# Optimization experiments

Measured on AMD Instinct MI355X. Metric: run time of the kernel, lower is better.

## Reference

```python
import jax, jax.numpy as jnp
import numpy as np

NUM_PARAMS = 8          # number of generalized coordinates q
DIM = 2 * NUM_PARAMS    # state = (q, q_dot)
HID = 128               # hidden width of the Lagrangian MLP
BATCH = 4096


def _linear_init(key, fan_in, fan_out):
    # torch nn.Linear default init: U(-1/sqrt(fan_in), 1/sqrt(fan_in))
    lim = 1.0 / np.sqrt(fan_in)
    kw, kb = jax.random.split(key)
    W = jax.random.uniform(kw, (fan_out, fan_in), minval=-lim, maxval=lim, dtype=jnp.float32)
    b = jax.random.uniform(kb, (fan_out,), minval=-lim, maxval=lim, dtype=jnp.float32)
    return W, b


def setup_inputs() -> dict:
    key = jax.random.key(0)
    ks = jax.random.split(key, 6)
    W1, b1 = _linear_init(ks[0], DIM, HID)
    W2, b2 = _linear_init(ks[1], HID, HID)
    W3, b3 = _linear_init(ks[2], HID, HID)
    W4, b4 = _linear_init(ks[3], HID, HID)
    W5, b5 = _linear_init(ks[4], HID, 1)
    x = jax.random.normal(ks[5], (BATCH, DIM), dtype=jnp.float32)
    return {"x": x, "W1": W1, "b1": b1, "W2": W2, "b2": b2,
            "W3": W3, "b3": b3, "W4": W4, "b4": b4, "W5": W5, "b5": b5}


def reference(x, W1, b1, W2, b2, W3, b3, W4, b4, W5, b5):
    n = NUM_PARAMS

    def lagrangian(xs):  # xs: (DIM,) -> scalar L
        h = jax.nn.softplus(W1 @ xs + b1)
        h = jax.nn.softplus(W2 @ h + b2)
        h = jax.nn.softplus(W3 @ h + b3)
        h = jax.nn.softplus(W4 @ h + b4)
        return (W5 @ h + b5)[0]

    def per_sample(xs):
        J = jax.grad(lagrangian)(xs)            # (DIM,) = dL/dx
        H = jax.hessian(lagrangian)(xs)         # (DIM, DIM)
        A = J[:n]                               # dL/dq
        B = H[n:, n:]                           # d2L/dq_dot dq_dot
        C = H[n:, :n]                           # d2L/dq_dot dq
        # q_ddot = pinv(B) @ (dL/dq - d2L/dq_dot dq @ q_dot)
        return jnp.linalg.pinv(B) @ (A - C @ xs[n:])

    return jax.vmap(per_sample)(x)              # (BATCH, NUM_PARAMS)
```

## Files before the change

kernel.cpp:

```cpp
#include <hip/hip_runtime.h>
#include <math.h>

#define NPAR 8
#define DIM  16
#define HID  128
#define BATCH 4096
#define VSTRF 132
#define NVEC 9

typedef float v2f __attribute__((ext_vector_type(2)));

__device__ float g_wsf[6*HID*HID + HID*DIM];

__device__ __forceinline__ float sigf(float z){ return 1.0f/(1.0f+__expf(-z)); }
__device__ __forceinline__ float spf(float z){ return fmaxf(z,0.0f)+log1pf(__expf(-fabsf(z))); }
__device__ __forceinline__ int posf(int jo, int kr){
  return (((kr>>6)*16 + ((kr&63)>>2))*4 + (jo>>5))*128 + (jo&31)*4 + (kr&3);
}

__global__ void pack_weights(const float* __restrict__ W1, const float* __restrict__ W2,
                             const float* __restrict__ W3, const float* __restrict__ W4) {
  int t = blockIdx.x*blockDim.x + threadIdx.x;
  if (t < 3*HID*HID) {
    int m = t/(HID*HID); int r = t%(HID*HID);
    int j = r/HID, k = r%HID;
    const float* W = (m==0)?W2:((m==1)?W3:W4);
    float w = W[j*HID+k];
    float* PF = g_wsf + m*2*HID*HID;
    float* PB = PF + HID*HID;
    PF[posf(j,k)] = w;
    PB[posf(k,j)] = w;
  } else {
    int r = t - 3*HID*HID;
    if (r < HID*DIM) {
      int k = r/DIM, m2 = r%DIM;
      g_wsf[6*HID*HID + (k>>2)*(DIM*4) + m2*4 + (k&3)] = W1[k*DIM+m2];
    }
  }
}

__device__ __forceinline__ void gemv9f32(const float* __restrict__ Wbase,
    const float* __restrict__ bin, int o, int kh, float* zA, float* zB) {
  const float4* Wq = (const float4*)Wbase;
  const float* hb = bin + kh*64;
  v2f acc[4][NVEC];
#pragma unroll
  for (int jj=0;jj<4;++jj)
#pragma unroll
    for (int v=0;v<NVEC;++v) acc[jj][v] = (v2f){0.0f, 0.0f};
#pragma unroll 4
  for (int q=0;q<16;++q){
    int base = ((kh*16+q)*4)*32 + o;
    float4 w0 = Wq[base], w1 = Wq[base+32], w2 = Wq[base+64], w3 = Wq[base+96];
    v2f w0a={w0.x,w0.y}, w0b={w0.z,w0.w};
    v2f w1a={w1.x,w1.y}, w1b={w1.z,w1.w};
    v2f w2a={w2.x,w2.y}, w2b={w2.z,w2.w};
    v2f w3a={w3.x,w3.y}, w3b={w3.z,w3.w};
#pragma unroll
    for (int v=0;v<NVEC;++v){
      float4 h = *((const float4*)(hb + v*VSTRF + 4*q));
      v2f ha={h.x,h.y}, hc={h.z,h.w};
      acc[0][v] = __builtin_elementwise_fma(w0b,hc, __builtin_elementwise_fma(w0a,ha, acc[0][v]));
      acc[1][v] = __builtin_elementwise_fma(w1b,hc, __builtin_elementwise_fma(w1a,ha, acc[1][v]));
      acc[2][v] = __builtin_elementwise_fma(w2b,hc, __builtin_elementwise_fma(w2a,ha, acc[2][v]));
      acc[3][v] = __builtin_elementwise_fma(w3b,hc, __builtin_elementwise_fma(w3a,ha, acc[3][v]));
    }
  }
#pragma unroll
  for (int v=0;v<NVEC;++v){
    float u0 = acc[0][v].x + acc[0][v].y;
    float u1 = acc[1][v].x + acc[1][v].y;
    float u2 = acc[2][v].x + acc[2][v].y;
    float u3 = acc[3][v].x + acc[3][v].y;
    u0 += __shfl_xor(u0,32);
    u1 += __shfl_xor(u1,32);
    u2 += __shfl_xor(u2,32);
    u3 += __shfl_xor(u3,32);
    zA[v] = kh ? u2 : u0;
    zB[v] = kh ? u3 : u1;
  }
}

__global__ __launch_bounds__(64)
__attribute__((amdgpu_waves_per_eu(2)))
void lnn_main(const float* __restrict__ x, const float* __restrict__ W1,
              const float* __restrict__ b1, const float* __restrict__ b2,
              const float* __restrict__ b3, const float* __restrict__ b4,
              const float* __restrict__ W5, float* __restrict__ out) {
  const int l  = threadIdx.x;
  const int o  = l & 31;
  const int kh = l >> 5;
  const int ja = o + 64*kh;
  const int jb = ja + 32;
  const int s  = blockIdx.x;

  __shared__ __align__(16) float buf[NVEC*VSTRF];
  __shared__ float xs[16];

  if (l < DIM) xs[l] = x[s*DIM + l];
  __syncthreads();

  const float4* W1v = (const float4*)W1;
  float s1a, s1b;
  float w1af[8], w1bf[8];
  {
    float4 a0 = W1v[ja*4+0], a1 = W1v[ja*4+1], a2 = W1v[ja*4+2], a3 = W1v[ja*4+3];
    float4 c0 = W1v[jb*4+0], c1 = W1v[jb*4+1], c2 = W1v[jb*4+2], c3 = W1v[jb*4+3];
    float z1a = b1[ja], z1b = b1[jb];
    z1a = fmaf(a0.x, xs[0],  z1a); z1a = fmaf(a0.y, xs[1],  z1a);
    z1a = fmaf(a0.z, xs[2],  z1a); z1a = fmaf(a0.w, xs[3],  z1a);
    z1a = fmaf(a1.x, xs[4],  z1a); z1a = fmaf(a1.y, xs[5],  z1a);
    z1a = fmaf(a1.z, xs[6],  z1a); z1a = fmaf(a1.w, xs[7],  z1a);
    z1a = fmaf(a2.x, xs[8],  z1a); z1a = fmaf(a2.y, xs[9],  z1a);
    z1a = fmaf(a2.z, xs[10], z1a); z1a = fmaf(a2.w, xs[11], z1a);
    z1a = fmaf(a3.x, xs[12], z1a); z1a = fmaf(a3.y, xs[13], z1a);
    z1a = fmaf(a3.z, xs[14], z1a); z1a = fmaf(a3.w, xs[15], z1a);
    z1b = fmaf(c0.x, xs[0],  z1b); z1b = fmaf(c0.y, xs[1],  z1b);
    z1b = fmaf(c0.z, xs[2],  z1b); z1b = fmaf(c0.w, xs[3],  z1b);
    z1b = fmaf(c1.x, xs[4],  z1b); z1b = fmaf(c1.y, xs[5],  z1b);
    z1b = fmaf(c1.z, xs[6],  z1b); z1b = fmaf(c1.w, xs[7],  z1b);
    z1b = fmaf(c2.x, xs[8],  z1b); z1b = fmaf(c2.y, xs[9],  z1b);
    z1b = fmaf(c2.z, xs[10], z1b); z1b = fmaf(c2.w, xs[11], z1b);
    z1b = fmaf(c3.x, xs[12], z1b); z1b = fmaf(c3.y, xs[13], z1b);
    z1b = fmaf(c3.z, xs[14], z1b); z1b = fmaf(c3.w, xs[15], z1b);
    s1a = sigf(z1a); s1b = sigf(z1b);
    buf[ja] = spf(z1a); buf[jb] = spf(z1b);
    w1af[0]=a2.x; w1af[1]=a2.y; w1af[2]=a2.z; w1af[3]=a2.w;
    w1af[4]=a3.x; w1af[5]=a3.y; w1af[6]=a3.z; w1af[7]=a3.w;
    w1bf[0]=c2.x; w1bf[1]=c2.y; w1bf[2]=c2.z; w1bf[3]=c2.w;
    w1bf[4]=c3.x; w1bf[5]=c3.y; w1bf[6]=c3.z; w1bf[7]=c3.w;
#pragma unroll
    for (int i=0;i<8;++i){
      buf[(1+i)*VSTRF + ja] = s1a*w1af[i];
      buf[(1+i)*VSTRF + jb] = s1b*w1bf[i];
    }
  }
  __syncthreads();

  float zA[NVEC], zB[NVEC];

  gemv9f32(g_wsf + 0, buf, o, kh, zA, zB);
  float z2a = zA[0] + b2[ja], z2b = zB[0] + b2[jb];
  float t2a[8], t2b[8];
#pragma unroll
  for (int i=0;i<8;++i){ t2a[i]=zA[1+i]; t2b[i]=zB[1+i]; }
  float s2a = sigf(z2a), s2b = sigf(z2b);
  __syncthreads();
  buf[ja] = spf(z2a); buf[jb] = spf(z2b);
#pragma unroll
  for (int i=0;i<8;++i){
    buf[(1+i)*VSTRF + ja] = s2a*zA[1+i];
    buf[(1+i)*VSTRF + jb] = s2b*zB[1+i];
  }
  __syncthreads();

  gemv9f32(g_wsf + 32768, buf, o, kh, zA, zB);
  float z3a = zA[0] + b3[ja], z3b = zB[0] + b3[jb];
  float t3a[8], t3b[8];
#pragma unroll
  for (int i=0;i<8;++i){ t3a[i]=zA[1+i]; t3b[i]=zB[1+i]; }
  float s3a = sigf(z3a), s3b = sigf(z3b);
  __syncthreads();
  buf[ja] = spf(z3a); buf[jb] = spf(z3b);
#pragma unroll
  for (int i=0;i<8;++i){
    buf[(1+i)*VSTRF + ja] = s3a*zA[1+i];
    buf[(1+i)*VSTRF + jb] = s3b*zB[1+i];
  }
  __syncthreads();

  gemv9f32(g_wsf + 65536, buf, o, kh, zA, zB);
  {
    float z4a = zA[0] + b4[ja], z4b = zB[0] + b4[jb];
    float w5a = W5[ja], w5b = W5[jb];
    float sa = sigf(z4a), sb = sigf(z4b);
    float ca = w5a*sa*(1.0f-sa), cb = w5b*sb*(1.0f-sb);
    __syncthreads();
    buf[ja] = w5a*sa; buf[jb] = w5b*sb;
#pragma unroll
    for (int i=0;i<8;++i){
      buf[(1+i)*VSTRF + ja] = ca*zA[1+i];
      buf[(1+i)*VSTRF + jb] = cb*zB[1+i];
    }
  }
  __syncthreads();

  gemv9f32(g_wsf + 81920, buf, o, kh, zA, zB);
  {
    float da = s3a*(1.0f-s3a)*zA[0], db = s3b*(1.0f-s3b)*zB[0];
    __syncthreads();
    buf[ja] = zA[0]*s3a; buf[jb] = zB[0]*s3b;
#pragma unroll
    for (int i=0;i<8;++i){
      buf[(1+i)*VSTRF + ja] = fmaf(zA[1+i], s3a, da*t3a[i]);
      buf[(1+i)*VSTRF + jb] = fmaf(zB[1+i], s3b, db*t3b[i]);
    }
  }
  __syncthreads();

  gemv9f32(g_wsf + 49152, buf, o, kh, zA, zB);
  {
    float da = s2a*(1.0f-s2a)*zA[0], db = s2b*(1.0f-s2b)*zB[0];
    __syncthreads();
    buf[ja] = zA[0]*s2a; buf[jb] = zB[0]*s2b;
#pragma unroll
    for (int i=0;i<8;++i){
      buf[(1+i)*VSTRF + ja] = fmaf(zA[1+i], s2a, da*t2a[i]);
      buf[(1+i)*VSTRF + jb] = fmaf(zB[1+i], s2b, db*t2b[i]);
    }
  }
  __syncthreads();

  gemv9f32(g_wsf + 16384, buf, o, kh, zA, zB);
  {
    float da = s1a*(1.0f-s1a)*zA[0], db = s1b*(1.0f-s1b)*zB[0];
    __syncthreads();
    buf[ja] = zA[0]*s1a; buf[jb] = zB[0]*s1b;
#pragma unroll
    for (int i=0;i<8;++i){
      buf[(1+i)*VSTRF + ja] = fmaf(zA[1+i], s1a, da*w1af[i]);
      buf[(1+i)*VSTRF + jb] = fmaf(zB[1+i], s1b, db*w1bf[i]);
    }
  }
  __syncthreads();

  float hA, hB, hJ;
  {
    const int m = l & 15, d = l >> 4;
    const float4* P1 = (const float4*)(g_wsf + 98304);
    v2f aA={0.0f,0.0f}, aB={0.0f,0.0f}, aJ={0.0f,0.0f};
#pragma unroll 4
    for (int q=0; q<32; ++q){
      float4 wq = P1[q*DIM + m];
      v2f wa={wq.x,wq.y}, wb={wq.z,wq.w};
      float4 u0 = *((const float4*)(buf + (1+d)*VSTRF + 4*q));
      float4 u1 = *((const float4*)(buf + (5+d)*VSTRF + 4*q));
      float4 gg = *((const float4*)(buf + 4*q));
      aA = __builtin_elementwise_fma(wb,(v2f){u0.z,u0.w}, __builtin_elementwise_fma(wa,(v2f){u0.x,u0.y}, aA));
      aB = __builtin_elementwise_fma(wb,(v2f){u1.z,u1.w}, __builtin_elementwise_fma(wa,(v2f){u1.x,u1.y}, aB));
      aJ = __builtin_elementwise_fma(wb,(v2f){gg.z,gg.w}, __builtin_elementwise_fma(wa,(v2f){gg.x,gg.y}, aJ));
    }
    hA = aA.x + aA.y;
    hB = aB.x + aB.y;
    hJ = aJ.x + aJ.y;
  }

  {
    const int r = l >> 3, c = l & 7;
    float BvA = __shfl(hA, ((r&3)*16) + 8 + c);
    float BvB = __shfl(hB, ((r&3)*16) + 8 + c);
    float Bv  = (r < 4) ? BvA : BvB;
    float CrA = __shfl(hA, ((r&3)*16) + c);
    float CrB = __shfl(hB, ((r&3)*16) + c);
    float Cr  = (r < 4) ? CrA : CrB;
    float Jr  = __shfl(hJ, r);
    float p0 = Cr * xs[8 + c];
    p0 += __shfl_xor(p0, 1); p0 += __shfl_xor(p0, 2); p0 += __shfl_xor(p0, 4);
    float rhs = Jr - p0;

    float Bt = __shfl(Bv, c*8 + r);
    float Am = 0.5f*(Bv + Bt);
    float Vm = (r == c) ? 1.0f : 0.0f;

    for (int sweep = 0; sweep < 4; ++sweep) {
#pragma unroll
      for (int rr = 0; rr < 7; ++rr) {
        int pc = (c == 7) ? rr : ((c == rr) ? 7 : (2*rr + 7 - c) % 7);
        int cp = min(c, pc), cq = max(c, pc);
        float App = __shfl(Am, cp*8+cp);
        float Aqq = __shfl(Am, cq*8+cq);
        float Apq = __shfl(Am, cp*8+cq);
        float tau = (Aqq - App) / (2.0f*Apq);
        float tt  = (tau >= 0.0f ? 1.0f : -1.0f) / (fabsf(tau) + sqrtf(1.0f + tau*tau));
        float cth = 1.0f / sqrtf(1.0f + tt*tt);
        float sth = tt * cth;
        if (fabsf(Apq) < 1e-30f) { cth = 1.0f; sth = 0.0f; }
        float cthr = __shfl(cth, r*8+r);
        float sthr = __shfl(sth, r*8+r);
        float Arp = __shfl(Am, r*8+cp);
        float Arq = __shfl(Am, r*8+cq);
        float colv = (c == cp) ? (cth*Arp - sth*Arq) : (sth*Arp + cth*Arq);
        int pr2 = (r == 7) ? rr : ((r == rr) ? 7 : (2*rr + 7 - r) % 7);
        int rp = min(r, pr2), rq = max(r, pr2);
        float Mpc = __shfl(colv, rp*8+c);
        float Mqc = __shfl(colv, rq*8+c);
        Am = (r == rp) ? (cthr*Mpc - sthr*Mqc) : (sthr*Mpc + cthr*Mqc);
        float Vrp = __shfl(Vm, r*8+cp);
        float Vrq = __shfl(Vm, r*8+cq);
        Vm = (c == cp) ? (cth*Vrp - sth*Vrq) : (sth*Vrp + cth*Vrq);
      }
    }

    float lam_c = __shfl(Am, c*8 + c);
    float adiag = (r == c) ? fabsf(Am) : 0.0f;
#pragma unroll
    for (int off = 32; off; off >>= 1) adiag = fmaxf(adiag, __shfl_xor(adiag, off));
    float cutoff = 9.5367431640625e-06f * adiag;

    float pr = Vm * rhs;
    pr += __shfl_xor(pr, 8); pr += __shfl_xor(pr, 16); pr += __shfl_xor(pr, 32);
    float w = (fabsf(lam_c) > cutoff) ? (pr / lam_c) : 0.0f;
    float yr = Vm * w;
    yr += __shfl_xor(yr, 1); yr += __shfl_xor(yr, 2); yr += __shfl_xor(yr, 4);
    if (c == 0) out[s*NPAR + r] = yr;
  }
}

extern "C" void kernel_launch(void* const* d_in, const int* in_sizes, int n_in,
                              void* d_out, int out_size, void* d_ws, size_t ws_size,
                              hipStream_t stream) {
  (void)in_sizes; (void)n_in; (void)out_size; (void)d_ws; (void)ws_size;
  const float* x  = (const float*)d_in[0];
  const float* W1 = (const float*)d_in[1];
  const float* b1 = (const float*)d_in[2];
  const float* W2 = (const float*)d_in[3];
  const float* b2 = (const float*)d_in[4];
  const float* W3 = (const float*)d_in[5];
  const float* b3 = (const float*)d_in[6];
  const float* W4 = (const float*)d_in[7];
  const float* b4 = (const float*)d_in[8];
  const float* W5 = (const float*)d_in[9];
  float* out = (float*)d_out;

  pack_weights<<<200, 256, 0, stream>>>(W1, W2, W3, W4);
  lnn_main<<<BATCH, 64, 0, stream>>>(x, W1, b1, b2, b3, b4, W5, out);
}
```

Baseline: 225.9 us.

## Replace FP32 GEMV chain with split-bf16 MFMA emulating FP32 precision

The per-sample forward and tangent/backward GEMVs move from scalar packed-FP32 FMAs to MFMA 16x16x32 bf16 instructions. Both weights and activations are split into three bf16 parts (hi/mid/lo), and six cross-product MFMAs per tile approximate FP32 accuracy. Weights are pre-packed into MFMA fragment layout, and activations are staged in LDS as three bf16 planes. This aims to use matrix-core throughput instead of VALU. The cost is six times the MFMA work, extra conversion overhead, and a risk of small precision differences.

```diff
diff --git a/kernel.cpp b/kernel.cpp
--- a/kernel.cpp
+++ b/kernel.cpp
@@ -5,256 +5,292 @@
 #define DIM  16
 #define HID  128
 #define BATCH 4096
-#define VSTRF 132
-#define NVEC 9
-
-typedef float v2f __attribute__((ext_vector_type(2)));
-
-__device__ float g_wsf[6*HID*HID + HID*DIM];
+
+typedef __attribute__((ext_vector_type(8))) short short8;
+typedef __attribute__((ext_vector_type(4))) float f32x4;
+
+__device__ __align__(16) unsigned short g_fr[301056];
 
 __device__ __forceinline__ float sigf(float z){ return 1.0f/(1.0f+__expf(-z)); }
 __device__ __forceinline__ float spf(float z){ return fmaxf(z,0.0f)+log1pf(__expf(-fabsf(z))); }
-__device__ __forceinline__ int posf(int jo, int kr){
-  return (((kr>>6)*16 + ((kr&63)>>2))*4 + (jo>>5))*128 + (jo&31)*4 + (kr&3);
-}
+__device__ __forceinline__ unsigned short bf16rne(float v){
+  unsigned u = __float_as_uint(v);
+  u += 0x7FFFu + ((u>>16)&1u);
+  return (unsigned short)(u>>16);
+}
+__device__ __forceinline__ float bf2f(unsigned short h){ return __uint_as_float(((unsigned)h)<<16); }
 
 __global__ void pack_weights(const float* __restrict__ W1, const float* __restrict__ W2,
-                             const float* __restrict__ W3, const float* __restrict__ W4) {
+                             const float* __restrict__ W3, const float* __restrict__ W4){
   int t = blockIdx.x*blockDim.x + threadIdx.x;
-  if (t < 3*HID*HID) {
-    int m = t/(HID*HID); int r = t%(HID*HID);
-    int j = r/HID, k = r%HID;
-    const float* W = (m==0)?W2:((m==1)?W3:W4);
-    float w = W[j*HID+k];
-    float* PF = g_wsf + m*2*HID*HID;
-    float* PB = PF + HID*HID;
-    PF[posf(j,k)] = w;
-    PB[posf(k,j)] = w;
+  if (t >= 301056) return;
+  float val; int p;
+  if (t < 294912){
+    int slot = t/49152, r = t%49152;
+    p = r/16384; int r2 = r%16384;
+    int c = r2/4096, r3 = r2%4096;
+    int mt = r3/512, r4 = r3%512;
+    int lane = r4/8, i = r4%8;
+    int m = mt*16 + (lane&15);
+    int k = c*32 + (lane>>4)*8 + i;
+    const float* W = (slot>>1)==0 ? W2 : ((slot>>1)==1 ? W3 : W4);
+    val = ((slot&1)==0) ? W[m*HID + k] : W[k*HID + m];
   } else {
-    int r = t - 3*HID*HID;
-    if (r < HID*DIM) {
-      int k = r/DIM, m2 = r%DIM;
-      g_wsf[6*HID*HID + (k>>2)*(DIM*4) + m2*4 + (k&3)] = W1[k*DIM+m2];
-    }
-  }
-}
-
-__device__ __forceinline__ void gemv9f32(const float* __restrict__ Wbase,
-    const float* __restrict__ bin, int o, int kh, float* zA, float* zB) {
-  const float4* Wq = (const float4*)Wbase;
-  const float* hb = bin + kh*64;
-  v2f acc[4][NVEC];
-#pragma unroll
-  for (int jj=0;jj<4;++jj)
-#pragma unroll
-    for (int v=0;v<NVEC;++v) acc[jj][v] = (v2f){0.0f, 0.0f};
-#pragma unroll 4
-  for (int q=0;q<16;++q){
-    int base = ((kh*16+q)*4)*32 + o;
-    float4 w0 = Wq[base], w1 = Wq[base+32], w2 = Wq[base+64], w3 = Wq[base+96];
-    v2f w0a={w0.x,w0.y}, w0b={w0.z,w0.w};
-    v2f w1a={w1.x,w1.y}, w1b={w1.z,w1.w};
-    v2f w2a={w2.x,w2.y}, w2b={w2.z,w2.w};
-    v2f w3a={w3.x,w3.y}, w3b={w3.z,w3.w};
-#pragma unroll
-    for (int v=0;v<NVEC;++v){
-      float4 h = *((const float4*)(hb + v*VSTRF + 4*q));
-      v2f ha={h.x,h.y}, hc={h.z,h.w};
-      acc[0][v] = __builtin_elementwise_fma(w0b,hc, __builtin_elementwise_fma(w0a,ha, acc[0][v]));
-      acc[1][v] = __builtin_elementwise_fma(w1b,hc, __builtin_elementwise_fma(w1a,ha, acc[1][v]));
-      acc[2][v] = __builtin_elementwise_fma(w2b,hc, __builtin_elementwise_fma(w2a,ha, acc[2][v]));
-      acc[3][v] = __builtin_elementwise_fma(w3b,hc, __builtin_elementwise_fma(w3a,ha, acc[3][v]));
-    }
-  }
-#pragma unroll
-  for (int v=0;v<NVEC;++v){
-    float u0 = acc[0][v].x + acc[0][v].y;
-    float u1 = acc[1][v].x + acc[1][v].y;
-    float u2 = acc[2][v].x + acc[2][v].y;
-    float u3 = acc[3][v].x + acc[3][v].y;
-    u0 += __shfl_xor(u0,32);
-    u1 += __shfl_xor(u1,32);
-    u2 += __shfl_xor(u2,32);
-    u3 += __shfl_xor(u3,32);
-    zA[v] = kh ? u2 : u0;
-    zB[v] = kh ? u3 : u1;
+    int idx = t - 294912;
+    p = idx/2048; int r = idx%2048;
+    int c = r/512, r2 = r%512;
+    int lane = r2/8, i = r2%8;
+    int md = lane&15;
+    int k = c*32 + (lane>>4)*8 + i;
+    val = W1[k*DIM + md];
+  }
+  unsigned short h = bf16rne(val); float rem  = val - bf2f(h);
+  unsigned short m2 = bf16rne(rem); float rem2 = rem - bf2f(m2);
+  unsigned short lo = bf16rne(rem2);
+  g_fr[t] = (p==0)? h : (p==1)? m2 : lo;
+}
+
+template<int NMT, int PSTR, int CSTR>
+__device__ __forceinline__ void gemv_mfma(const unsigned short* __restrict__ fr,
+                                          const unsigned short* __restrict__ hl,
+                                          int lane, f32x4* acc){
+  const int n = lane & 15, kg = lane >> 4;
+#pragma unroll
+  for (int mt=0; mt<NMT; ++mt) acc[mt] = (f32x4){0.f,0.f,0.f,0.f};
+#pragma unroll
+  for (int c=0;c<4;++c){
+    const int hoff = n*136 + c*32 + kg*8;
+    short8 Bh = *(const short8*)(hl + hoff);
+    short8 Bm = *(const short8*)(hl + 2176 + hoff);
+    short8 Bl = *(const short8*)(hl + 4352 + hoff);
+#pragma unroll
+    for (int mt=0; mt<NMT; ++mt){
+      const unsigned short* ab = fr + c*CSTR + mt*512 + lane*8;
+      short8 Ah = *(const short8*)(ab);
+      short8 Am = *(const short8*)(ab + PSTR);
+      short8 Al = *(const short8*)(ab + 2*PSTR);
+      acc[mt] = __builtin_amdgcn_mfma_f32_16x16x32_bf16(Ah,Bh,acc[mt],0,0,0);
+      acc[mt] = __builtin_amdgcn_mfma_f32_16x16x32_bf16(Ah,Bm,acc[mt],0,0,0);
+      acc[mt] = __builtin_amdgcn_mfma_f32_16x16x32_bf16(Am,Bh,acc[mt],0,0,0);
+      acc[mt] = __builtin_amdgcn_mfma_f32_16x16x32_bf16(Ah,Bl,acc[mt],0,0,0);
+      acc[mt] = __builtin_amdgcn_mfma_f32_16x16x32_bf16(Am,Bm,acc[mt],0,0,0);
+      acc[mt] = __builtin_amdgcn_mfma_f32_16x16x32_bf16(Al,Bh,acc[mt],0,0,0);
+    }
+  }
+}
+
+__device__ __forceinline__ void write4(unsigned short* base, float v0, float v1, float v2, float v3){
+#pragma unroll
+  for (int p=0;p<3;++p){
+    unsigned short h0=bf16rne(v0), h1=bf16rne(v1), h2=bf16rne(v2), h3=bf16rne(v3);
+    uint2 w; w.x = (unsigned)h0 | ((unsigned)h1<<16); w.y = (unsigned)h2 | ((unsigned)h3<<16);
+    *(uint2*)(base + p*2176) = w;
+    v0 -= bf2f(h0); v1 -= bf2f(h1); v2 -= bf2f(h2); v3 -= bf2f(h3);
   }
 }
 
 __global__ __launch_bounds__(64)
-__attribute__((amdgpu_waves_per_eu(2)))
 void lnn_main(const float* __restrict__ x, const float* __restrict__ W1,
               const float* __restrict__ b1, const float* __restrict__ b2,
               const float* __restrict__ b3, const float* __restrict__ b4,
-              const float* __restrict__ W5, float* __restrict__ out) {
-  const int l  = threadIdx.x;
-  const int o  = l & 31;
-  const int kh = l >> 5;
-  const int ja = o + 64*kh;
-  const int jb = ja + 32;
-  const int s  = blockIdx.x;
-
-  __shared__ __align__(16) float buf[NVEC*VSTRF];
-  __shared__ float xs[16];
-
-  if (l < DIM) xs[l] = x[s*DIM + l];
-  __syncthreads();
-
-  const float4* W1v = (const float4*)W1;
-  float s1a, s1b;
-  float w1af[8], w1bf[8];
-  {
+              const float* __restrict__ W5, float* __restrict__ out){
+  const int l = threadIdx.x;
+  const int sid = blockIdx.x;
+  const int n = l & 15, kg = l >> 4;
+  const int l48 = l & 48;
+
+  __shared__ __align__(16) unsigned short Hl[6528];
+  __shared__ float sA[3*128];
+  __shared__ float xsl[16];
+
+  if (l < DIM) xsl[l] = x[sid*DIM + l];
+  __syncthreads();
+
+  {
+    const int o = l & 31, kh = l >> 5;
+    const int ja = o + 64*kh, jb = ja + 32;
+    const float4* W1v = (const float4*)W1;
     float4 a0 = W1v[ja*4+0], a1 = W1v[ja*4+1], a2 = W1v[ja*4+2], a3 = W1v[ja*4+3];
     float4 c0 = W1v[jb*4+0], c1 = W1v[jb*4+1], c2 = W1v[jb*4+2], c3 = W1v[jb*4+3];
     float z1a = b1[ja], z1b = b1[jb];
-    z1a = fmaf(a0.x, xs[0],  z1a); z1a = fmaf(a0.y, xs[1],  z1a);
-    z1a = fmaf(a0.z, xs[2],  z1a); z1a = fmaf(a0.w, xs[3],  z1a);
-    z1a = fmaf(a1.x, xs[4],  z1a); z1a = fmaf(a1.y, xs[5],  z1a);
-    z1a = fmaf(a1.z, xs[6],  z1a); z1a = fmaf(a1.w, xs[7],  z1a);
-    z1a = fmaf(a2.x, xs[8],  z1a); z1a = fmaf(a2.y, xs[9],  z1a);
-    z1a = fmaf(a2.z, xs[10], z1a); z1a = fmaf(a2.w, xs[11], z1a);
-    z1a = fmaf(a3.x, xs[12], z1a); z1a = fmaf(a3.y, xs[13], z1a);
-    z1a = fmaf(a3.z, xs[14], z1a); z1a = fmaf(a3.w, xs[15], z1a);
-    z1b = fmaf(c0.x, xs[0],  z1b); z1b = fmaf(c0.y, xs[1],  z1b);
-    z1b = fmaf(c0.z, xs[2],  z1b); z1b = fmaf(c0.w, xs[3],  z1b);
-    z1b = fmaf(c1.x, xs[4],  z1b); z1b = fmaf(c1.y, xs[5],  z1b);
-    z1b = fmaf(c1.z, xs[6],  z1b); z1b = fmaf(c1.w, xs[7],  z1b);
-    z1b = fmaf(c2.x, xs[8],  z1b); z1b = fmaf(c2.y, xs[9],  z1b);
-    z1b = fmaf(c2.z, xs[10], z1b); z1b = fmaf(c2.w, xs[11], z1b);
-    z1b = fmaf(c3.x, xs[12], z1b); z1b = fmaf(c3.y, xs[13], z1b);
-    z1b = fmaf(c3.z, xs[14], z1b); z1b = fmaf(c3.w, xs[15], z1b);
-    s1a = sigf(z1a); s1b = sigf(z1b);
-    buf[ja] = spf(z1a); buf[jb] = spf(z1b);
-    w1af[0]=a2.x; w1af[1]=a2.y; w1af[2]=a2.z; w1af[3]=a2.w;
-    w1af[4]=a3.x; w1af[5]=a3.y; w1af[6]=a3.z; w1af[7]=a3.w;
-    w1bf[0]=c2.x; w1bf[1]=c2.y; w1bf[2]=c2.z; w1bf[3]=c2.w;
-    w1bf[4]=c3.x; w1bf[5]=c3.y; w1bf[6]=c3.z; w1bf[7]=c3.w;
-#pragma unroll
-    for (int i=0;i<8;++i){
-      buf[(1+i)*VSTRF + ja] = s1a*w1af[i];
-      buf[(1+i)*VSTRF + jb] = s1b*w1bf[i];
-    }
-  }
-  __syncthreads();
-
-  float zA[NVEC], zB[NVEC];
-
-  gemv9f32(g_wsf + 0, buf, o, kh, zA, zB);
-  float z2a = zA[0] + b2[ja], z2b = zB[0] + b2[jb];
-  float t2a[8], t2b[8];
-#pragma unroll
-  for (int i=0;i<8;++i){ t2a[i]=zA[1+i]; t2b[i]=zB[1+i]; }
-  float s2a = sigf(z2a), s2b = sigf(z2b);
-  __syncthreads();
-  buf[ja] = spf(z2a); buf[jb] = spf(z2b);
-#pragma unroll
-  for (int i=0;i<8;++i){
-    buf[(1+i)*VSTRF + ja] = s2a*zA[1+i];
-    buf[(1+i)*VSTRF + jb] = s2b*zB[1+i];
-  }
-  __syncthreads();
-
-  gemv9f32(g_wsf + 32768, buf, o, kh, zA, zB);
-  float z3a = zA[0] + b3[ja], z3b = zB[0] + b3[jb];
-  float t3a[8], t3b[8];
-#pragma unroll
-  for (int i=0;i<8;++i){ t3a[i]=zA[1+i]; t3b[i]=zB[1+i]; }
-  float s3a = sigf(z3a), s3b = sigf(z3b);
-  __syncthreads();
-  buf[ja] = spf(z3a); buf[jb] = spf(z3b);
-#pragma unroll
-  for (int i=0;i<8;++i){
-    buf[(1+i)*VSTRF + ja] = s3a*zA[1+i];
-    buf[(1+i)*VSTRF + jb] = s3b*zB[1+i];
-  }
-  __syncthreads();
-
-  gemv9f32(g_wsf + 65536, buf, o, kh, zA, zB);
-  {
-    float z4a = zA[0] + b4[ja], z4b = zB[0] + b4[jb];
-    float w5a = W5[ja], w5b = W5[jb];
-    float sa = sigf(z4a), sb = sigf(z4b);
-    float ca = w5a*sa*(1.0f-sa), cb = w5b*sb*(1.0f-sb);
-    __syncthreads();
-    buf[ja] = w5a*sa; buf[jb] = w5b*sb;
-#pragma unroll
-    for (int i=0;i<8;++i){
-      buf[(1+i)*VSTRF + ja] = ca*zA[1+i];
-      buf[(1+i)*VSTRF + jb] = cb*zB[1+i];
-    }
-  }
-  __syncthreads();
-
-  gemv9f32(g_wsf + 81920, buf, o, kh, zA, zB);
-  {
-    float da = s3a*(1.0f-s3a)*zA[0], db = s3b*(1.0f-s3b)*zB[0];
-    __syncthreads();
-    buf[ja] = zA[0]*s3a; buf[jb] = zB[0]*s3b;
-#pragma unroll
-    for (int i=0;i<8;++i){
-      buf[(1+i)*VSTRF + ja] = fmaf(zA[1+i], s3a, da*t3a[i]);
-      buf[(1+i)*VSTRF + jb] = fmaf(zB[1+i], s3b, db*t3b[i]);
-    }
-  }
-  __syncthreads();
-
-  gemv9f32(g_wsf + 49152, buf, o, kh, zA, zB);
-  {
-    float da = s2a*(1.0f-s2a)*zA[0], db = s2b*(1.0f-s2b)*zB[0];
-    __syncthreads();
-    buf[ja] = zA[0]*s2a; buf[jb] = zB[0]*s2b;
-#pragma unroll
-    for (int i=0;i<8;++i){
-      buf[(1+i)*VSTRF + ja] = fmaf(zA[1+i], s2a, da*t2a[i]);
-      buf[(1+i)*VSTRF + jb] = fmaf(zB[1+i], s2b, db*t2b[i]);
-    }
-  }
-  __syncthreads();
-
-  gemv9f32(g_wsf + 16384, buf, o, kh, zA, zB);
-  {
-    float da = s1a*(1.0f-s1a)*zA[0], db = s1b*(1.0f-s1b)*zB[0];
-    __syncthreads();
-    buf[ja] = zA[0]*s1a; buf[jb] = zB[0]*s1b;
-#pragma unroll
-    for (int i=0;i<8;++i){
-      buf[(1+i)*VSTRF + ja] = fmaf(zA[1+i], s1a, da*w1af[i]);
-      buf[(1+i)*VSTRF + jb] = fmaf(zB[1+i], s1b, db*w1bf[i]);
-    }
-  }
-  __syncthreads();
-
-  float hA, hB, hJ;
-  {
-    const int m = l & 15, d = l >> 4;
-    const float4* P1 = (const float4*)(g_wsf + 98304);
-    v2f aA={0.0f,0.0f}, aB={0.0f,0.0f}, aJ={0.0f,0.0f};
-#pragma unroll 4
-    for (int q=0; q<32; ++q){
-      float4 wq = P1[q*DIM + m];
-      v2f wa={wq.x,wq.y}, wb={wq.z,wq.w};
-      float4 u0 = *((const float4*)(buf + (1+d)*VSTRF + 4*q));
-      float4 u1 = *((const float4*)(buf + (5+d)*VSTRF + 4*q));
-      float4 gg = *((const float4*)(buf + 4*q));
-      aA = __builtin_elementwise_fma(wb,(v2f){u0.z,u0.w}, __builtin_elementwise_fma(wa,(v2f){u0.x,u0.y}, aA));
-      aB = __builtin_elementwise_fma(wb,(v2f){u1.z,u1.w}, __builtin_elementwise_fma(wa,(v2f){u1.x,u1.y}, aB));
-      aJ = __builtin_elementwise_fma(wb,(v2f){gg.z,gg.w}, __builtin_elementwise_fma(wa,(v2f){gg.x,gg.y}, aJ));
-    }
-    hA = aA.x + aA.y;
-    hB = aB.x + aB.y;
-    hJ = aJ.x + aJ.y;
-  }
+    z1a = fmaf(a0.x, xsl[0],  z1a); z1a = fmaf(a0.y, xsl[1],  z1a);
+    z1a = fmaf(a0.z, xsl[2],  z1a); z1a = fmaf(a0.w, xsl[3],  z1a);
+    z1a = fmaf(a1.x, xsl[4],  z1a); z1a = fmaf(a1.y, xsl[5],  z1a);
+    z1a = fmaf(a1.z, xsl[6],  z1a); z1a = fmaf(a1.w, xsl[7],  z1a);
+    z1a = fmaf(a2.x, xsl[8],  z1a); z1a = fmaf(a2.y, xsl[9],  z1a);
+    z1a = fmaf(a2.z, xsl[10], z1a); z1a = fmaf(a2.w, xsl[11], z1a);
+    z1a = fmaf(a3.x, xsl[12], z1a); z1a = fmaf(a3.y, xsl[13], z1a);
+    z1a = fmaf(a3.z, xsl[14], z1a); z1a = fmaf(a3.w, xsl[15], z1a);
+    z1b = fmaf(c0.x, xsl[0],  z1b); z1b = fmaf(c0.y, xsl[1],  z1b);
+    z1b = fmaf(c0.z, xsl[2],  z1b); z1b = fmaf(c0.w, xsl[3],  z1b);
+    z1b = fmaf(c1.x, xsl[4],  z1b); z1b = fmaf(c1.y, xsl[5],  z1b);
+    z1b = fmaf(c1.z, xsl[6],  z1b); z1b = fmaf(c1.w, xsl[7],  z1b);
+    z1b = fmaf(c2.x, xsl[8],  z1b); z1b = fmaf(c2.y, xsl[9],  z1b);
+    z1b = fmaf(c2.z, xsl[10], z1b); z1b = fmaf(c2.w, xsl[11], z1b);
+    z1b = fmaf(c3.x, xsl[12], z1b); z1b = fmaf(c3.y, xsl[13], z1b);
+    z1b = fmaf(c3.z, xsl[14], z1b); z1b = fmaf(c3.w, xsl[15], z1b);
+    float s1a = sigf(z1a), s1b = sigf(z1b);
+    sA[ja] = s1a; sA[jb] = s1b;
+    float wa[8] = {a2.x,a2.y,a2.z,a2.w,a3.x,a3.y,a3.z,a3.w};
+    float wb[8] = {c2.x,c2.y,c2.z,c2.w,c3.x,c3.y,c3.z,c3.w};
+    float vA[9], vB[9];
+    vA[0] = spf(z1a); vB[0] = spf(z1b);
+#pragma unroll
+    for (int i=0;i<8;++i){ vA[1+i] = s1a*wa[i]; vB[1+i] = s1b*wb[i]; }
+#pragma unroll
+    for (int v=0;v<9;++v){
+      float ra = vA[v], rb = vB[v];
+#pragma unroll
+      for (int p=0;p<3;++p){
+        unsigned short ha = bf16rne(ra); Hl[p*2176 + v*136 + ja] = ha; ra -= bf2f(ha);
+        unsigned short hb = bf16rne(rb); Hl[p*2176 + v*136 + jb] = hb; rb -= bf2f(hb);
+      }
+    }
+  }
+  __syncthreads();
+
+  f32x4 acc[8];
+  float t2c[8][4], t3c[8][4];
+
+  gemv_mfma<8,16384,4096>(g_fr + 0*49152, Hl, l, acc);
+  {
+    const float4* bv = (const float4*)b2;
+#pragma unroll
+    for (int mt=0; mt<8; ++mt){
+      float4 bias = bv[mt*4+kg];
+      float ov[4];
+#pragma unroll
+      for (int reg=0; reg<4; ++reg){
+        float c0 = __shfl(acc[mt][reg], l48);
+        float z  = c0 + ((const float*)&bias)[reg];
+        float s  = sigf(z);
+        t2c[mt][reg] = acc[mt][reg];
+        ov[reg] = (n==0) ? spf(z) : s*acc[mt][reg];
+        if (n==0) sA[128 + mt*16 + kg*4 + reg] = s;
+      }
+      if (n<9) write4(Hl + n*136 + mt*16 + kg*4, ov[0],ov[1],ov[2],ov[3]);
+    }
+  }
+  __syncthreads();
+
+  gemv_mfma<8,16384,4096>(g_fr + 2*49152, Hl, l, acc);
+  {
+    const float4* bv = (const float4*)b3;
+#pragma unroll
+    for (int mt=0; mt<8; ++mt){
+      float4 bias = bv[mt*4+kg];
+      float ov[4];
+#pragma unroll
+      for (int reg=0; reg<4; ++reg){
+        float c0 = __shfl(acc[mt][reg], l48);
+        float z  = c0 + ((const float*)&bias)[reg];
+        float s  = sigf(z);
+        t3c[mt][reg] = acc[mt][reg];
+        ov[reg] = (n==0) ? spf(z) : s*acc[mt][reg];
+        if (n==0) sA[256 + mt*16 + kg*4 + reg] = s;
+      }
+      if (n<9) write4(Hl + n*136 + mt*16 + kg*4, ov[0],ov[1],ov[2],ov[3]);
+    }
+  }
+  __syncthreads();
+
+  gemv_mfma<8,16384,4096>(g_fr + 4*49152, Hl, l, acc);
+  {
+    const float4* bv  = (const float4*)b4;
+    const float4* w5v = (const float4*)W5;
+#pragma unroll
+    for (int mt=0; mt<8; ++mt){
+      float4 bias = bv[mt*4+kg];
+      float4 w5q  = w5v[mt*4+kg];
+      float ov[4];
+#pragma unroll
+      for (int reg=0; reg<4; ++reg){
+        float c0 = __shfl(acc[mt][reg], l48);
+        float z  = c0 + ((const float*)&bias)[reg];
+        float s  = sigf(z);
+        float w5r = ((const float*)&w5q)[reg];
+        ov[reg] = (n==0) ? w5r*s : (w5r*s*(1.0f-s))*acc[mt][reg];
+      }
+      if (n<9) write4(Hl + n*136 + mt*16 + kg*4, ov[0],ov[1],ov[2],ov[3]);
+    }
+  }
+  __syncthreads();
+
+  gemv_mfma<8,16384,4096>(g_fr + 5*49152, Hl, l, acc);
+  {
+#pragma unroll
+    for (int mt=0; mt<8; ++mt){
+      float ov[4];
+#pragma unroll
+      for (int reg=0; reg<4; ++reg){
+        int j = mt*16 + kg*4 + reg;
+        float g   = __shfl(acc[mt][reg], l48);
+        float sld = sA[256 + j];
+        float d   = sld*(1.0f-sld)*g;
+        ov[reg] = (n==0) ? g*sld : fmaf(acc[mt][reg], sld, d*t3c[mt][reg]);
+      }
+      if (n<9) write4(Hl + n*136 + mt*16 + kg*4, ov[0],ov[1],ov[2],ov[3]);
+    }
+  }
+  __syncthreads();
+
+  gemv_mfma<8,16384,4096>(g_fr + 3*49152, Hl, l, acc);
+  {
+#pragma unroll
+    for (int mt=0; mt<8; ++mt){
+      float ov[4];
+#pragma unroll
+      for (int reg=0; reg<4; ++reg){
+        int j = mt*16 + kg*4 + reg;
+        float g   = __shfl(acc[mt][reg], l48);
+        float sld = sA[128 + j];
+        float d   = sld*(1.0f-sld)*g;
+        ov[reg] = (n==0) ? g*sld : fmaf(acc[mt][reg], sld, d*t2c[mt][reg]);
+      }
+      if (n<9) write4(Hl + n*136 + mt*16 + kg*4, ov[0],ov[1],ov[2],ov[3]);
+    }
+  }
+  __syncthreads();
+
+  gemv_mfma<8,16384,4096>(g_fr + 1*49152, Hl, l, acc);
+  {
+    const int col = (n>=1 && n<9) ? (7+n) : 7;
+#pragma unroll
+    for (int mt=0; mt<8; ++mt){
+      float ov[4];
+#pragma unroll
+      for (int reg=0; reg<4; ++reg){
+        int j = mt*16 + kg*4 + reg;
+        float g   = __shfl(acc[mt][reg], l48);
+        float sld = sA[j];
+        float d   = sld*(1.0f-sld)*g;
+        float w1c = W1[j*DIM + col];
+        ov[reg] = (n==0) ? g*sld : fmaf(acc[mt][reg], sld, d*w1c);
+      }
+      if (n<9) write4(Hl + n*136 + mt*16 + kg*4, ov[0],ov[1],ov[2],ov[3]);
+    }
+  }
+  __syncthreads();
+
+  f32x4 a9[1];
+  gemv_mfma<1,2048,512>(g_fr + 294912, Hl, l, a9);
+  float q0 = a9[0][0], q1 = a9[0][1], q2 = a9[0][2], q3 = a9[0][3];
 
   {
     const int r = l >> 3, c = l & 7;
-    float BvA = __shfl(hA, ((r&3)*16) + 8 + c);
-    float BvB = __shfl(hB, ((r&3)*16) + 8 + c);
-    float Bv  = (r < 4) ? BvA : BvB;
-    float CrA = __shfl(hA, ((r&3)*16) + c);
-    float CrB = __shfl(hB, ((r&3)*16) + c);
-    float Cr  = (r < 4) ? CrA : CrB;
-    float Jr  = __shfl(hJ, r);
-    float p0 = Cr * xs[8 + c];
+    int srcB = ((8+c)>>2)*16 + 1 + r;
+    float g0=__shfl(q0,srcB), g1=__shfl(q1,srcB), g2=__shfl(q2,srcB), g3=__shfl(q3,srcB);
+    int rb = c & 3;
+    float Bv = rb==0?g0: rb==1?g1: rb==2?g2: g3;
+    int srcC = (c>>2)*16 + 1 + r;
+    float h0=__shfl(q0,srcC), h1=__shfl(q1,srcC), h2=__shfl(q2,srcC), h3=__shfl(q3,srcC);
+    float Cv = rb==0?h0: rb==1?h1: rb==2?h2: h3;
+    int srcJ = (r>>2)*16;
+    float e0=__shfl(q0,srcJ), e1=__shfl(q1,srcJ), e2=__shfl(q2,srcJ), e3=__shfl(q3,srcJ);
+    int rj = r & 3;
+    float Jr = rj==0?e0: rj==1?e1: rj==2?e2: e3;
+
+    float p0 = Cv * xsl[8 + c];
     p0 += __shfl_xor(p0, 1); p0 += __shfl_xor(p0, 2); p0 += __shfl_xor(p0, 4);
     float rhs = Jr - p0;
 
@@ -302,7 +338,7 @@
     float w = (fabsf(lam_c) > cutoff) ? (pr / lam_c) : 0.0f;
     float yr = Vm * w;
     yr += __shfl_xor(yr, 1); yr += __shfl_xor(yr, 2); yr += __shfl_xor(yr, 4);
-    if (c == 0) out[s*NPAR + r] = yr;
+    if (c == 0) out[sid*NPAR + r] = yr;
   }
 }
 
@@ -322,6 +358,6 @@
   const float* W5 = (const float*)d_in[9];
   float* out = (float*)d_out;
 
-  pack_weights<<<200, 256, 0, stream>>>(W1, W2, W3, W4);
+  pack_weights<<<1176, 256, 0, stream>>>(W1, W2, W3, W4);
   lnn_main<<<BATCH, 64, 0, stream>>>(x, W1, b1, b2, b3, b4, W5, out);
 }
```

Result: slower. 320.0 us (+41.7%).
